# Optimization experiments

Hardware: AMD Instinct MI355X
Metric: run time of the kernel (lower is better)

The kernel has to match this reference:

```python
import jax, jax.numpy as jnp
import numpy as np

# BERT-base geometry
B, N, H, DH = 4, 512, 12, 64
HID = H * DH            # 768
E = 65536               # total edges (~avg degree 32)
NREL = 64               # relation vocabulary


def setup_inputs() -> dict:
    key = jax.random.key(0)
    ks = jax.random.split(key, 12)
    node_states = jax.random.normal(ks[0], (B, N, HID), jnp.float32)
    b = jax.random.randint(ks[1], (E,), 0, B)
    hn = jax.random.randint(ks[2], (E,), 0, N)
    tn = jax.random.randint(ks[3], (E,), 0, N)
    r = jax.random.randint(ks[4], (E,), 0, NREL)
    edge_indices = jnp.stack([b, hn, tn, r]).astype(jnp.int32)  # (4, E)
    node_type_ids = jnp.zeros((B, N), jnp.int32)  # unused by this subclass
    sc = 0.02
    Wq = jax.random.normal(ks[5], (HID, HID), jnp.float32) * sc
    bq = jnp.zeros((HID,), jnp.float32)
    Wk = jax.random.normal(ks[6], (HID, HID), jnp.float32) * sc
    bk = jnp.zeros((HID,), jnp.float32)
    Wv = jax.random.normal(ks[7], (HID, HID), jnp.float32) * sc
    bv = jnp.zeros((HID,), jnp.float32)
    # relation matrix embeddings: one (DH, DH) matrix per relation id
    rel_emb = jnp.eye(DH, dtype=jnp.float32)[None] + jax.random.normal(ks[8], (NREL, DH, DH), jnp.float32) * sc
    return {"node_states": node_states, "edge_indices": edge_indices,
            "node_type_ids": node_type_ids, "Wq": Wq, "bq": bq,
            "Wk": Wk, "bk": bk, "Wv": Wv, "bv": bv, "rel_emb": rel_emb}


def reference(node_states, edge_indices, node_type_ids, Wq, bq, Wk, bk, Wv, bv, rel_emb):
    Bq, Nn, hid = node_states.shape
    # dense QKV projections (torch Linear: y = x @ W^T + b)
    Q = node_states @ Wq.T + bq
    K = node_states @ Wk.T + bk
    V = (node_states @ Wv.T + bv).reshape(Bq, Nn, H, DH)  # (B,N,H,D)
    be, he, te, re = edge_indices  # each (E,)
    # per-edge gathers
    Qe = Q[be, he].reshape(-1, H, DH)   # (E,H,D)
    Ke = K[be, te].reshape(-1, H, DH)   # (E,H,D)
    Re = rel_emb[re]                     # (E,D,D) relation matrix per edge
    # Q projected through relation matrix, then inner product with K per head
    Qp = jnp.einsum('ehd,edk->ehk', Qe, Re)
    logits = jnp.einsum('ehd,ehd->eh', Qp, Ke) / jnp.sqrt(jnp.float32(DH))  # (E,H)
    # sparse softmax over tail nodes: segment = (batch, head_node)
    seg = be * Nn + he
    nseg = Bq * Nn
    m = jax.ops.segment_max(logits, seg, num_segments=nseg)      # (BN,H)
    ex = jnp.exp(logits - m[seg])
    denom = jax.ops.segment_sum(ex, seg, num_segments=nseg)      # (BN,H)
    p = ex / denom[seg]                                          # (E,H)
    # dropout prob = 0.0 (deterministic reference)
    # aggregate: out[b,i,h,:] = sum_edges p_e * V[b, tail_e, h, :]
    contrib = p[:, :, None] * V[be, te]                          # (E,H,D)
    out = jax.ops.segment_sum(contrib, seg, num_segments=nseg)   # (BN,H,D)
    return out.reshape(Bq, Nn, H * DH)
```

## Files before the change

### kernel.cpp

```cpp
#include <hip/hip_runtime.h>
#include <hip/hip_bf16.h>

#define NB   4
#define NN   512
#define NH   12
#define DHD  64
#define HID  768
#define NE   65536
#define NSEG 2048
#define NREL 64
#define LGS  16
#define SCAP 128
#define NSUB2 8
#define RSUB (NREL * NSUB2)
#define RCAP 256
#define RLY2 12
#define POISON 0xAAAAAAAAu

typedef short bf16x8 __attribute__((ext_vector_type(8)));
typedef float f32x4  __attribute__((ext_vector_type(4)));
typedef unsigned short u16x8 __attribute__((ext_vector_type(8)));

__device__ __forceinline__ unsigned short f2bf(float f) {
    __hip_bfloat16 h = __float2bfloat16(f);
    return *reinterpret_cast<unsigned short*>(&h);
}
__device__ __forceinline__ float bf2f(unsigned short s) {
    return __int_as_float(((int)s) << 16);
}
__device__ __forceinline__ int unpz(int v) {
    return (int)((unsigned)v - POISON);
}

#define NQKV 576
__global__ __launch_bounds__(256, 4) void qkv_scatter_kernel(
    const float* __restrict__ Xf,
    const float* __restrict__ Wq, const float* __restrict__ Wk,
    const float* __restrict__ Wv,
    const float* __restrict__ bq, const float* __restrict__ bk,
    const float* __restrict__ bv,
    unsigned short* __restrict__ Qh, unsigned short* __restrict__ Kh,
    unsigned short* __restrict__ Vh,
    const int* __restrict__ ei,
    int* __restrict__ cursor, int* __restrict__ rcursor,
    int* __restrict__ s_te, int* __restrict__ s_pkr)
{
    __shared__ __align__(16) char smem[64 * 132 * 4];
    const int tid = threadIdx.x;

    if (blockIdx.x >= NQKV) {
        const int e = (blockIdx.x - NQKV) * 256 + tid;
        const int b  = ei[e];
        const int hn = ei[NE + e];
        const int tn = ei[2 * NE + e];
        const int rr = ei[3 * NE + e];
        const int seg = b * NN + hn;
        const int slot = unpz(atomicAdd(&cursor[seg], 1)) & (SCAP - 1);
        const int pos  = seg * SCAP + slot;
        s_te[pos] = tn;
        const int rsub = rr * NSUB2 + ((e >> 8) & (NSUB2 - 1));
        const int rj = unpz(atomicAdd(&rcursor[rsub], 1)) & (RCAP - 1);
        int2 pv2; pv2.x = (seg << 9) | tn; pv2.y = pos;
        ((int2*)s_pkr)[rsub * RCAP + rj] = pv2;
        return;
    }

    const int gb  = blockIdx.x;
    const int bid = (gb & 7) * 72 + (gb >> 3);
    const int z   = bid / 192;
    const int rem = bid - z * 192;
    const int by  = rem / 6;
    const int bx  = rem - by * 6;
    const float* Wf = (z == 0) ? Wq : ((z == 1) ? Wk : Wv);
    const float* bias = (z == 0) ? bq : ((z == 1) ? bk : bv);

    const int n0 = bx * 128;
    const int m0 = by * 64;
    const int lane = tid & 63;
    const int wave = tid >> 6;
    const int wm = wave >> 1, wn = wave & 1;

    unsigned short* As = (unsigned short*)smem;
    unsigned short* Bs = (unsigned short*)(smem + 8192);
    float* Cs = (float*)smem;

    f32x4 acc[2][4];
    #pragma unroll
    for (int a = 0; a < 2; ++a)
        #pragma unroll
        for (int b2 = 0; b2 < 4; ++b2) acc[a][b2] = (f32x4){0.f, 0.f, 0.f, 0.f};

    const int ml = lane & 15;
    const int q4 = lane >> 4;

    int offA[2], offB[4];
    #pragma unroll
    for (int i = 0; i < 2; ++i) {
        const int idx = i * 256 + tid;
        const int row = idx >> 3;
        const int kq  = (idx & 7) ^ (row & 7);
        offA[i] = (m0 + row) * HID + kq * 8;
    }
    #pragma unroll
    for (int i = 0; i < 4; ++i) {
        const int idx = i * 256 + tid;
        const int row = idx >> 3;
        const int kq  = (idx & 7) ^ (row & 7);
        offB[i] = (n0 + row) * HID + kq * 8;
    }

    float4 a0[2], a1[2], b0[4], b1[4];
    #pragma unroll
    for (int i = 0; i < 2; ++i) {
        const float4* s = (const float4*)(Xf + offA[i]);
        a0[i] = s[0]; a1[i] = s[1];
    }
    #pragma unroll
    for (int i = 0; i < 4; ++i) {
        const float4* s = (const float4*)(Wf + offB[i]);
        b0[i] = s[0]; b1[i] = s[1];
    }

    for (int k0 = 0; k0 < HID; k0 += 64) {
        #pragma unroll
        for (int i = 0; i < 2; ++i) {
            u16x8 r8;
            r8[0] = f2bf(a0[i].x); r8[1] = f2bf(a0[i].y);
            r8[2] = f2bf(a0[i].z); r8[3] = f2bf(a0[i].w);
            r8[4] = f2bf(a1[i].x); r8[5] = f2bf(a1[i].y);
            r8[6] = f2bf(a1[i].z); r8[7] = f2bf(a1[i].w);
            *(u16x8*)(As + (i * 256 + tid) * 8) = r8;
        }
        #pragma unroll
        for (int i = 0; i < 4; ++i) {
            u16x8 r8;
            r8[0] = f2bf(b0[i].x); r8[1] = f2bf(b0[i].y);
            r8[2] = f2bf(b0[i].z); r8[3] = f2bf(b0[i].w);
            r8[4] = f2bf(b1[i].x); r8[5] = f2bf(b1[i].y);
            r8[6] = f2bf(b1[i].z); r8[7] = f2bf(b1[i].w);
            *(u16x8*)(Bs + (i * 256 + tid) * 8) = r8;
        }
        if (k0 + 64 < HID) {
            #pragma unroll
            for (int i = 0; i < 2; ++i) {
                const float4* s = (const float4*)(Xf + offA[i] + k0 + 64);
                a0[i] = s[0]; a1[i] = s[1];
            }
            #pragma unroll
            for (int i = 0; i < 4; ++i) {
                const float4* s = (const float4*)(Wf + offB[i] + k0 + 64);
                b0[i] = s[0]; b1[i] = s[1];
            }
        }
        __syncthreads();

        #pragma unroll
        for (int ks = 0; ks < 2; ++ks) {
            bf16x8 af[2], bfr[4];
            #pragma unroll
            for (int t = 0; t < 2; ++t) {
                const int ar = wm * 32 + t * 16 + ml;
                const int ac = (ks * 4 + q4) ^ (ar & 7);
                af[t] = *(const bf16x8*)(As + ar * 64 + ac * 8);
            }
            #pragma unroll
            for (int t = 0; t < 4; ++t) {
                const int br = wn * 64 + t * 16 + ml;
                const int bc = (ks * 4 + q4) ^ (br & 7);
                bfr[t] = *(const bf16x8*)(Bs + br * 64 + bc * 8);
            }
            #pragma unroll
            for (int mt = 0; mt < 2; ++mt)
                #pragma unroll
                for (int nt = 0; nt < 4; ++nt)
                    acc[mt][nt] = __builtin_amdgcn_mfma_f32_16x16x32_bf16(
                        af[mt], bfr[nt], acc[mt][nt], 0, 0, 0);
        }
        __syncthreads();
    }

    #pragma unroll
    for (int mt = 0; mt < 2; ++mt)
        #pragma unroll
        for (int nt = 0; nt < 4; ++nt)
            #pragma unroll
            for (int rg = 0; rg < 4; ++rg)
                Cs[(wm * 32 + mt * 16 + q4 * 4 + rg) * 132 +
                   wn * 64 + nt * 16 + ml] = acc[mt][nt][rg];
    __syncthreads();

    unsigned short* Y = (z == 0) ? Qh : ((z == 1) ? Kh : Vh);
    #pragma unroll
    for (int it = 0; it < 4; ++it) {
        const int id  = tid + it * 256;
        const int row = id >> 4;
        const int cg  = id & 15;
        const float* cp = Cs + row * 132 + cg * 8;
        const float4 cA = *(const float4*)cp;
        const float4 cB = *(const float4*)(cp + 4);
        const float* bp = bias + n0 + cg * 8;
        const float4 bA = *(const float4*)bp;
        const float4 bB = *(const float4*)(bp + 4);
        const size_t o = (size_t)(m0 + row) * HID + n0 + cg * 8;
        u16x8 r;
        r[0] = f2bf(cA.x + bA.x); r[1] = f2bf(cA.y + bA.y);
        r[2] = f2bf(cA.z + bA.z); r[3] = f2bf(cA.w + bA.w);
        r[4] = f2bf(cB.x + bB.x); r[5] = f2bf(cB.y + bB.y);
        r[6] = f2bf(cB.z + bB.z); r[7] = f2bf(cB.w + bB.w);
        *(u16x8*)&Y[o] = r;
    }
}

__global__ __launch_bounds__(256) void rel_logits(
    const unsigned short* __restrict__ Qh, const unsigned short* __restrict__ Kh,
    const float* __restrict__ rel,
    const int* __restrict__ rcursor, const int* __restrict__ s_pkr,
    float* __restrict__ Lg)
{
    const int rs = blockIdx.x;
    int cnt = unpz(rcursor[rs]);
    cnt = (cnt < 0) ? 0 : ((cnt > RCAP) ? RCAP : cnt);
    const int rows = cnt * NH;
    if ((int)blockIdx.y * 256 >= rows) return;
    const int r = rs >> 3;
    const int tid = threadIdx.x;
    const int lane = tid & 63;
    const int wave = tid >> 6;

    __shared__ int qb[256], kb[256], oi[256];
    __shared__ float QpS[4][16][68];
    __shared__ __align__(16) unsigned short frS[4096];

    {
        const float* Rg = rel + (size_t)r * 4096;
        #pragma unroll
        for (int it = 0; it < 4; ++it) {
            const int i4 = it * 256 + tid;
            const float4 v4 = ((const float4*)Rg)[i4];
            const int d  = i4 >> 4;
            const int c0 = (i4 & 15) * 4;
            const int ks = d >> 5, q4 = (d >> 3) & 3, j = d & 7;
            const float vv[4] = {v4.x, v4.y, v4.z, v4.w};
            #pragma unroll
            for (int e = 0; e < 4; ++e) {
                const int c = c0 + e, nt = c >> 4, n = c & 15;
                frS[((ks * 4 + nt) * 64 + q4 * 16 + n) * 8 + j] = f2bf(vv[e]);
            }
        }
    }
    __syncthreads();
    bf16x8 bfrag[2][4];
    #pragma unroll
    for (int ks = 0; ks < 2; ++ks)
        #pragma unroll
        for (int nt = 0; nt < 4; ++nt)
            bfrag[ks][nt] = *(const bf16x8*)(frS + ((ks * 4 + nt) * 64 + lane) * 8);

    for (int t0 = blockIdx.y * 256; t0 < rows; t0 += RLY2 * 256) {
        __syncthreads();
        {
            const int rowid = t0 + tid;
            if (rowid < rows) {
                const int el = rowid / 12;
                const int h  = rowid - el * 12;
                const int2 v = ((const int2*)s_pkr)[rs * RCAP + el];
                const int pos = v.y & (NSEG * SCAP - 1);
                const int sg  = (v.x >> 9) & (NSEG - 1);
                const int te  = v.x & (NN - 1);
                qb[tid] = sg * HID + h * 64;
                kb[tid] = ((sg & ~(NN - 1)) + te) * HID + h * 64;
                oi[tid] = pos * LGS + h;
            } else { qb[tid] = 0; kb[tid] = 0; oi[tid] = -1; }
        }
        __syncthreads();

        const int rw = lane >> 2, ch = (lane & 3) * 16;
        bf16x8 kv0[4], kv1[4];
        #pragma unroll
        for (int gi = 0; gi < 4; ++gi) {
            const int kbase = kb[(wave + gi * 4) * 16 + rw];
            kv0[gi] = *(const bf16x8*)(Kh + kbase + ch);
            kv1[gi] = *(const bf16x8*)(Kh + kbase + ch + 8);
        }

        #pragma unroll
        for (int gi = 0; gi < 4; ++gi) {
            const int g = wave + gi * 4;
            const int m = lane & 15, q4 = lane >> 4;
            const int qbase = qb[g * 16 + m];
            f32x4 cfr[4] = {{0,0,0,0},{0,0,0,0},{0,0,0,0},{0,0,0,0}};
            #pragma unroll
            for (int ks = 0; ks < 2; ++ks) {
                const bf16x8 afr = *(const bf16x8*)(Qh + qbase + ks * 32 + q4 * 8);
                #pragma unroll
                for (int nt = 0; nt < 4; ++nt)
                    cfr[nt] = __builtin_amdgcn_mfma_f32_16x16x32_bf16(
                        afr, bfrag[ks][nt], cfr[nt], 0, 0, 0);
            }
            #pragma unroll
            for (int nt = 0; nt < 4; ++nt)
                #pragma unroll
                for (int rg = 0; rg < 4; ++rg)
                    QpS[wave][q4 * 4 + rg][nt * 16 + m] = cfr[nt][rg];

            const int rowid2 = g * 16 + rw;
            float s = 0.f;
            #pragma unroll
            for (int i = 0; i < 8; ++i) {
                s = fmaf(QpS[wave][rw][ch + i],     bf2f((unsigned short)kv0[gi][i]), s);
                s = fmaf(QpS[wave][rw][ch + 8 + i], bf2f((unsigned short)kv1[gi][i]), s);
            }
            s += __shfl_xor(s, 1, 64);
            s += __shfl_xor(s, 2, 64);
            if ((lane & 3) == 0) {
                const int o = oi[rowid2];
                if (o >= 0) Lg[o] = __expf(s * 0.125f);
            }
        }
    }
}

__global__ __launch_bounds__(256) void seg_softmax_agg(
    const unsigned short* __restrict__ Vh, const float* __restrict__ Lg,
    const int* __restrict__ s_te,
    float* __restrict__ out,
    int* __restrict__ cursor, int* __restrict__ rcursor)
{
    const int seg  = blockIdx.x;
    const int tid  = threadIdx.x;
    int cnt = unpz(cursor[seg]);
    __syncthreads();
    if (tid == 0) {
        cursor[seg] = (int)POISON;
        if (seg < RSUB) rcursor[seg] = (int)POISON;
    }
    cnt = (cnt < 0) ? 0 : ((cnt > SCAP) ? SCAP : cnt);
    const int base = seg * SCAP;
    const int lane = tid & 63;
    const int w    = tid >> 6;
    const int browbase = seg & ~(NN - 1);

    __shared__ int   te_s[64];
    __shared__ float pv[4][3][64];

    float l0 = 0.f, l1 = 0.f, l2 = 0.f;
    float acc0 = 0.f, acc1 = 0.f, acc2 = 0.f;

    for (int c0 = 0; c0 < cnt; c0 += 64) {
        const int cc = min(64, cnt - c0);
        __syncthreads();
        if (tid < 64)
            te_s[tid] = (tid < cc) ? (s_te[base + c0 + tid] & (NN - 1)) : 0;
        __syncthreads();

        float p0 = 0.f, p1 = 0.f, p2 = 0.f;
        if (lane < cc) {
            const float* Lp = Lg + (size_t)(base + c0 + lane) * LGS;
            p0 = Lp[w]; p1 = Lp[4 + w]; p2 = Lp[8 + w];
        }
        float s0 = p0, s1 = p1, s2 = p2;
        #pragma unroll
        for (int o = 1; o < 64; o <<= 1) {
            s0 += __shfl_xor(s0, o, 64);
            s1 += __shfl_xor(s1, o, 64);
            s2 += __shfl_xor(s2, o, 64);
        }
        l0 += s0; l1 += s1; l2 += s2;
        pv[w][0][lane] = p0; pv[w][1][lane] = p1; pv[w][2][lane] = p2;

        for (int j0 = 0; j0 < cc; j0 += 4) {
            float vb0[4], vb1[4], vb2[4];
            #pragma unroll
            for (int u = 0; u < 4; ++u) {
                const unsigned short* __restrict__ Vr =
                    Vh + (size_t)(browbase + te_s[(j0 + u) & 63]) * HID + lane;
                vb0[u] = bf2f(Vr[w * 64]);
                vb1[u] = bf2f(Vr[(4 + w) * 64]);
                vb2[u] = bf2f(Vr[(8 + w) * 64]);
            }
            #pragma unroll
            for (int u = 0; u < 4; ++u) {
                const int j = j0 + u;
                acc0 = fmaf(pv[w][0][j & 63], vb0[u], acc0);
                acc1 = fmaf(pv[w][1][j & 63], vb1[u], acc1);
                acc2 = fmaf(pv[w][2][j & 63], vb2[u], acc2);
            }
        }
    }

    float* Yo = out + (size_t)seg * HID;
    Yo[tid]       = (l0 > 0.f) ? acc0 / l0 : 0.f;
    Yo[tid + 256] = (l1 > 0.f) ? acc1 / l1 : 0.f;
    Yo[tid + 512] = (l2 > 0.f) ? acc2 / l2 : 0.f;
}

extern "C" void kernel_launch(void* const* d_in, const int* in_sizes, int n_in,
                              void* d_out, int out_size, void* d_ws, size_t ws_size,
                              hipStream_t stream)
{
    const float* X   = (const float*)d_in[0];
    const int*   EI  = (const int*)d_in[1];
    const float* Wq  = (const float*)d_in[3];
    const float* bq  = (const float*)d_in[4];
    const float* Wk  = (const float*)d_in[5];
    const float* bk  = (const float*)d_in[6];
    const float* Wv  = (const float*)d_in[7];
    const float* bv  = (const float*)d_in[8];
    const float* rel = (const float*)d_in[9];
    float* out = (float*)d_out;

    char* p = (char*)d_ws;
    unsigned short* Qh = (unsigned short*)p;  p += (size_t)NSEG * HID * 2;
    unsigned short* Kh = (unsigned short*)p;  p += (size_t)NSEG * HID * 2;
    unsigned short* Vh = (unsigned short*)p;  p += (size_t)NSEG * HID * 2;
    float* Lg = (float*)p;                    p += (size_t)NSEG * SCAP * LGS * 4;
    int* cursor   = (int*)p;                  p += NSEG * 4;
    int* rcursor  = (int*)p;                  p += RSUB * 4;
    int* s_te     = (int*)p;                  p += (size_t)NSEG * SCAP * 4;
    int* s_pkr    = (int*)p;                  p += (size_t)RSUB * RCAP * 8;

    qkv_scatter_kernel<<<NQKV + 256, 256, 0, stream>>>(
        X, Wq, Wk, Wv, bq, bk, bv, Qh, Kh, Vh,
        EI, cursor, rcursor, s_te, s_pkr);
    rel_logits<<<dim3(RSUB, RLY2), 256, 0, stream>>>(
        Qh, Kh, rel, rcursor, s_pkr, Lg);
    seg_softmax_agg<<<NSEG, 256, 0, stream>>>(
        Vh, Lg, s_te, out, cursor, rcursor);
}
```

Baseline: 165.2 us.

## Split fp32-to-bf16 cast into separate pass and stream GEMM tiles via global_load_lds

Adds a pre-pass kernel that converts X and the three weight matrices to bf16 in workspace, and fuses the edge-scatter work into that pass. The QKV GEMM then loads bf16 tiles directly into LDS with global_load_lds instead of loading fp32 into registers, converting, and storing to LDS. This removes the per-tile conversion and register staging inside the GEMM. In exchange it adds a kernel launch, an extra round trip through global memory for the bf16 copies, and the software register prefetch overlap is gone.

```diff
diff --git a/kernel.cpp b/kernel.cpp
--- a/kernel.cpp
+++ b/kernel.cpp
@@ -31,25 +31,25 @@
 __device__ __forceinline__ int unpz(int v) {
     return (int)((unsigned)v - POISON);
 }
-
-#define NQKV 576
-__global__ __launch_bounds__(256, 4) void qkv_scatter_kernel(
-    const float* __restrict__ Xf,
-    const float* __restrict__ Wq, const float* __restrict__ Wk,
-    const float* __restrict__ Wv,
-    const float* __restrict__ bq, const float* __restrict__ bk,
-    const float* __restrict__ bv,
-    unsigned short* __restrict__ Qh, unsigned short* __restrict__ Kh,
-    unsigned short* __restrict__ Vh,
+__device__ __forceinline__ void load_lds16(const void* g, void* l) {
+    __builtin_amdgcn_global_load_lds(
+        (const __attribute__((address_space(1))) unsigned int*)g,
+        (__attribute__((address_space(3))) unsigned int*)l, 16, 0, 0);
+}
+
+#define NX4 ((2048 * 768) / 4)
+#define NW4 ((768 * 768) / 4)
+#define NCAST ((NX4 + 3 * NW4) / 256)
+__global__ __launch_bounds__(256) void cast_scatter_kernel(
+    const float* __restrict__ X, const float* __restrict__ Wq,
+    const float* __restrict__ Wk, const float* __restrict__ Wv,
+    unsigned short* __restrict__ Xh, unsigned short* __restrict__ Wh,
     const int* __restrict__ ei,
     int* __restrict__ cursor, int* __restrict__ rcursor,
     int* __restrict__ s_te, int* __restrict__ s_pkr)
 {
-    __shared__ __align__(16) char smem[64 * 132 * 4];
-    const int tid = threadIdx.x;
-
-    if (blockIdx.x >= NQKV) {
-        const int e = (blockIdx.x - NQKV) * 256 + tid;
+    if (blockIdx.x >= NCAST) {
+        const int e = (blockIdx.x - NCAST) * 256 + threadIdx.x;
         const int b  = ei[e];
         const int hn = ei[NE + e];
         const int tn = ei[2 * NE + e];
@@ -64,6 +64,34 @@
         ((int2*)s_pkr)[rsub * RCAP + rj] = pv2;
         return;
     }
+    const int i = blockIdx.x * 256 + threadIdx.x;
+    float4 v;
+    ushort4* dst;
+    if (i < NX4) {
+        v = ((const float4*)X)[i];
+        dst = &((ushort4*)Xh)[i];
+    } else {
+        const int j = i - NX4;
+        const float* W = (j < NW4) ? Wq : ((j < 2 * NW4) ? Wk : Wv);
+        const int jj = (j < NW4) ? j : ((j < 2 * NW4) ? j - NW4 : j - 2 * NW4);
+        v = ((const float4*)W)[jj];
+        dst = &((ushort4*)Wh)[j];
+    }
+    ushort4 r;
+    r.x = f2bf(v.x); r.y = f2bf(v.y); r.z = f2bf(v.z); r.w = f2bf(v.w);
+    *dst = r;
+}
+
+#define NQKV 576
+__global__ __launch_bounds__(256) void qkv_kernel(
+    const unsigned short* __restrict__ Xh, const unsigned short* __restrict__ Wh,
+    const float* __restrict__ bq, const float* __restrict__ bk,
+    const float* __restrict__ bv,
+    unsigned short* __restrict__ Qh, unsigned short* __restrict__ Kh,
+    unsigned short* __restrict__ Vh)
+{
+    __shared__ __align__(16) char smem[64 * 132 * 4];
+    const int tid = threadIdx.x;
 
     const int gb  = blockIdx.x;
     const int bid = (gb & 7) * 72 + (gb >> 3);
@@ -71,7 +99,7 @@
     const int rem = bid - z * 192;
     const int by  = rem / 6;
     const int bx  = rem - by * 6;
-    const float* Wf = (z == 0) ? Wq : ((z == 1) ? Wk : Wv);
+    const unsigned short* W = Wh + (size_t)z * (768 * 768);
     const float* bias = (z == 0) ? bq : ((z == 1) ? bk : bv);
 
     const int n0 = bx * 128;
@@ -93,64 +121,25 @@
     const int ml = lane & 15;
     const int q4 = lane >> 4;
 
-    int offA[2], offB[4];
-    #pragma unroll
-    for (int i = 0; i < 2; ++i) {
-        const int idx = i * 256 + tid;
-        const int row = idx >> 3;
-        const int kq  = (idx & 7) ^ (row & 7);
-        offA[i] = (m0 + row) * HID + kq * 8;
-    }
-    #pragma unroll
-    for (int i = 0; i < 4; ++i) {
-        const int idx = i * 256 + tid;
-        const int row = idx >> 3;
-        const int kq  = (idx & 7) ^ (row & 7);
-        offB[i] = (n0 + row) * HID + kq * 8;
-    }
-
-    float4 a0[2], a1[2], b0[4], b1[4];
-    #pragma unroll
-    for (int i = 0; i < 2; ++i) {
-        const float4* s = (const float4*)(Xf + offA[i]);
-        a0[i] = s[0]; a1[i] = s[1];
-    }
-    #pragma unroll
-    for (int i = 0; i < 4; ++i) {
-        const float4* s = (const float4*)(Wf + offB[i]);
-        b0[i] = s[0]; b1[i] = s[1];
-    }
-
     for (int k0 = 0; k0 < HID; k0 += 64) {
+        __syncthreads();
         #pragma unroll
         for (int i = 0; i < 2; ++i) {
-            u16x8 r8;
-            r8[0] = f2bf(a0[i].x); r8[1] = f2bf(a0[i].y);
-            r8[2] = f2bf(a0[i].z); r8[3] = f2bf(a0[i].w);
-            r8[4] = f2bf(a1[i].x); r8[5] = f2bf(a1[i].y);
-            r8[6] = f2bf(a1[i].z); r8[7] = f2bf(a1[i].w);
-            *(u16x8*)(As + (i * 256 + tid) * 8) = r8;
+            const int slotb = i * 256 + wave * 64;
+            const int idx = slotb + lane;
+            const int row = idx >> 3;
+            const int kq  = (idx & 7) ^ (row & 7);
+            load_lds16(Xh + (size_t)(m0 + row) * HID + k0 + kq * 8,
+                       As + slotb * 8);
         }
         #pragma unroll
         for (int i = 0; i < 4; ++i) {
-            u16x8 r8;
-            r8[0] = f2bf(b0[i].x); r8[1] = f2bf(b0[i].y);
-            r8[2] = f2bf(b0[i].z); r8[3] = f2bf(b0[i].w);
-            r8[4] = f2bf(b1[i].x); r8[5] = f2bf(b1[i].y);
-            r8[6] = f2bf(b1[i].z); r8[7] = f2bf(b1[i].w);
-            *(u16x8*)(Bs + (i * 256 + tid) * 8) = r8;
-        }
-        if (k0 + 64 < HID) {
-            #pragma unroll
-            for (int i = 0; i < 2; ++i) {
-                const float4* s = (const float4*)(Xf + offA[i] + k0 + 64);
-                a0[i] = s[0]; a1[i] = s[1];
-            }
-            #pragma unroll
-            for (int i = 0; i < 4; ++i) {
-                const float4* s = (const float4*)(Wf + offB[i] + k0 + 64);
-                b0[i] = s[0]; b1[i] = s[1];
-            }
+            const int slotb = i * 256 + wave * 64;
+            const int idx = slotb + lane;
+            const int row = idx >> 3;
+            const int kq  = (idx & 7) ^ (row & 7);
+            load_lds16(W + (size_t)(n0 + row) * HID + k0 + kq * 8,
+                       Bs + slotb * 8);
         }
         __syncthreads();
 
@@ -176,9 +165,9 @@
                     acc[mt][nt] = __builtin_amdgcn_mfma_f32_16x16x32_bf16(
                         af[mt], bfr[nt], acc[mt][nt], 0, 0, 0);
         }
-        __syncthreads();
-    }
-
+    }
+
+    __syncthreads();
     #pragma unroll
     for (int mt = 0; mt < 2; ++mt)
         #pragma unroll
@@ -414,14 +403,17 @@
     unsigned short* Kh = (unsigned short*)p;  p += (size_t)NSEG * HID * 2;
     unsigned short* Vh = (unsigned short*)p;  p += (size_t)NSEG * HID * 2;
     float* Lg = (float*)p;                    p += (size_t)NSEG * SCAP * LGS * 4;
+    unsigned short* Xh = (unsigned short*)p;  p += (size_t)NB * NN * HID * 2;
+    unsigned short* Wh = (unsigned short*)p;  p += (size_t)3 * 768 * 768 * 2;
     int* cursor   = (int*)p;                  p += NSEG * 4;
     int* rcursor  = (int*)p;                  p += RSUB * 4;
     int* s_te     = (int*)p;                  p += (size_t)NSEG * SCAP * 4;
     int* s_pkr    = (int*)p;                  p += (size_t)RSUB * RCAP * 8;
 
-    qkv_scatter_kernel<<<NQKV + 256, 256, 0, stream>>>(
-        X, Wq, Wk, Wv, bq, bk, bv, Qh, Kh, Vh,
-        EI, cursor, rcursor, s_te, s_pkr);
+    cast_scatter_kernel<<<NCAST + 256, 256, 0, stream>>>(
+        X, Wq, Wk, Wv, Xh, Wh, EI, cursor, rcursor, s_te, s_pkr);
+    qkv_kernel<<<NQKV, 256, 0, stream>>>(
+        Xh, Wh, bq, bk, bv, Qh, Kh, Vh);
     rel_logits<<<dim3(RSUB, RLY2), 256, 0, stream>>>(
         Qh, Kh, rel, rcursor, s_pkr, Lg);
     seg_softmax_agg<<<NSEG, 256, 0, stream>>>(
```

New measurement: 171.6 us. 1.04x slower.
